# Optimization experiments

Hardware: AMD Instinct MI355X
Metric: run time of the kernel (lower is better)

The kernel has to match this reference:

```python
import jax, jax.numpy as jnp
import numpy as np

TARGET_RADIUS = 0.95
EPS = 1e-8

def _spectral_norm_wh(W_h, u):
    # Power iteration (3 steps) is done under no_grad in the original torch code,
    # so u, v are constants w.r.t. differentiation.
    Ws = jax.lax.stop_gradient(W_h)
    v = None
    for _ in range(3):
        v = Ws.T @ u
        v = v / (jnp.linalg.norm(v) + EPS)
        u = Ws @ v
        u = u / (jnp.linalg.norm(u) + EPS)
    sigma = jnp.abs(u @ W_h @ v)  # gradient flows through W_h here
    return W_h * (TARGET_RADIUS / (sigma + EPS))


def setup_inputs() -> dict:
    key = jax.random.key(0)
    kx, kwx, kwh, ku = jax.random.split(key, 4)
    T, B, D = 2048, 8, 1024
    x = jax.random.normal(kx, (T, B, D), dtype=jnp.float32)
    h0 = jnp.zeros((B, D), dtype=jnp.float32)
    W_x = jax.random.normal(kwx, (D, D), dtype=jnp.float32) * 0.02
    W_h = jax.random.normal(kwh, (D, D), dtype=jnp.float32) * (1.0 / np.sqrt(D))
    b = jnp.zeros((D,), dtype=jnp.float32)
    u = jax.random.normal(ku, (D,), dtype=jnp.float32)
    u = u / jnp.linalg.norm(u)
    return {"x": x, "h0": h0, "W_x": W_x, "W_h": W_h, "b": b, "u": u}


def reference(x, h0, W_x, W_h, b, u):
    # x: [T, B, D], h0: [B, D]
    Wh = _spectral_norm_wh(W_h, u)
    # Input projection is independent of the recurrence: one big GEMM.
    pre = jnp.einsum('tbd,ed->tbe', x, W_x) + b  # [T, B, D]

    def step(h_prev, p_t):
        h_new = p_t + h_prev @ Wh.T  # linear recurrence, no tanh
        return h_new, h_new

    _, hs = jax.lax.scan(step, h0, pre)  # hs: [T, B, D]
    h_all = jnp.concatenate([h0[None], hs], axis=0)  # [T+1, B, D]
    output = hs * (hs * jax.nn.sigmoid(hs))  # h * silu(h)
    return output, h_all
```

## Files before the change

kernel.cpp:

```cpp
#include <hip/hip_runtime.h>
#include <hip/hip_bf16.h>

#define DEV __device__ __forceinline__

typedef __bf16 bf16x8 __attribute__((ext_vector_type(8)));
typedef float  f32x4  __attribute__((ext_vector_type(4)));
typedef unsigned short u16;

DEV u16   f2b(float f) { __bf16 h = (__bf16)f; return __builtin_bit_cast(u16, h); }
DEV float b2f(u16 x)   { return __builtin_bit_cast(float, ((unsigned)x) << 16); }

DEV void gl_lds16(const u16* g, u16* l) {
  __builtin_amdgcn_global_load_lds((const __attribute__((address_space(1))) void*)g,
                                   (__attribute__((address_space(3))) void*)l, 16, 0, 0);
}

DEV long arow(int m, int S, int j) {
  if (S > 0)  return ((long)((m >> 3) * S + j)) * 8 + (m & 7);
  if (S == 0) return m;
  return m & 7;
}

struct ZCfg {
  const u16 *A0, *A1, *A2, *A3, *A4;
  const u16 *B0, *B1, *B2, *B3, *B4;
  int S0, J0, S1, J1, S2, J2, S3, J3, S4, J4;
  int nseg, mvalid, q, mode, ylim;
  const float* addc;
  const float* addf;
  const u16*   addb; int addS, addJ;
  float* outf;
  u16 *outb, *outbT, *outlo;
  u16* outm; int oS, oJ;
  u16 *glamH, *glamL;
  float *hall, *out0;
};
struct GArgs { ZCfg z0, z1, z2, z3; };

__global__ __launch_bounds__(256) void gU(GArgs ga)
{
  ZCfg c;
  switch (blockIdx.z) { case 0: c = ga.z0; break; case 1: c = ga.z1; break;
                        case 2: c = ga.z2; break; default: c = ga.z3; break; }

  int gx = gridDim.x;
  int fid = blockIdx.y * gx + blockIdx.x;
  int nwg = gx * gridDim.y;
  int idx = (c.ylim == (int)gridDim.y) ? ((fid & 7) * (nwg >> 3) + (fid >> 3))
                                       : fid;
  int mt = idx / gx, et = idx % gx;
  if (mt >= c.ylim) return;
  int m0 = mt << 6, e0 = et << 6;

  const int K = c.nseg << 10;
  int tid = threadIdx.x, lane = tid & 63, w = tid >> 6;
  int wrow = (w >> 1) << 5, wcol = (w & 1) << 5;

  __shared__ u16 As[2][8192], Bs[2][8192];
  f32x4 acc[2][2] = {};

  int rA[4], cA[4];
#pragma unroll
  for (int j = 0; j < 4; ++j) {
    int p = (j * 4 + w) * 1024 + lane * 16;
    int r = p >> 8, o = (p & 255) ^ ((r & 7) << 4);
    rA[j] = r; cA[j] = o >> 1;
  }
  auto seg = [&](int i, const u16*& A, int& S, int& J, const u16*& B) {
    switch (i) {
      case 0: A = c.A0; S = c.S0; J = c.J0; B = c.B0; break;
      case 1: A = c.A1; S = c.S1; J = c.J1; B = c.B1; break;
      case 2: A = c.A2; S = c.S2; J = c.J2; B = c.B2; break;
      case 3: A = c.A3; S = c.S3; J = c.J3; B = c.B3; break;
      default: A = c.A4; S = c.S4; J = c.J4; B = c.B4; break;
    }
  };
  auto stage = [&](int buf, int kt) {
    int si = kt >> 10, kl = kt & 1023;
    const u16 *A, *B; int S, J;
    seg(si, A, S, J, B);
#pragma unroll
    for (int j = 0; j < 4; ++j) {
      int grow = m0 + rA[j];
      gl_lds16(A + arow(grow, S, J) * 1024 + kl + cA[j], &As[buf][(j * 4 + w) * 512]);
    }
#pragma unroll
    for (int j = 0; j < 4; ++j)
      gl_lds16(B + (size_t)(e0 + rA[j]) * 1024 + kl + cA[j], &Bs[buf][(j * 4 + w) * 512]);
  };

  stage(0, 0);
  asm volatile("s_waitcnt vmcnt(0)" ::: "memory");
  __syncthreads();

  int buf = 0;
  for (int kt = 0; kt < K; kt += 128, buf ^= 1) {
    if (kt + 128 < K) stage(buf ^ 1, kt + 128);
#pragma unroll
    for (int ks = 0; ks < 4; ++ks) {
      int oa = ks * 64 + ((lane >> 4) << 4);
      bf16x8 af[2], bf[2];
#pragma unroll
      for (int s = 0; s < 2; ++s) {
        int ra = wrow + s * 16 + (lane & 15);
        int rb = wcol + s * 16 + (lane & 15);
        af[s] = *(const bf16x8*)((const char*)&As[buf][0] + ra * 256 + (oa ^ ((ra & 7) << 4)));
        bf[s] = *(const bf16x8*)((const char*)&Bs[buf][0] + rb * 256 + (oa ^ ((rb & 7) << 4)));
      }
#pragma unroll
      for (int ms = 0; ms < 2; ++ms)
#pragma unroll
        for (int ns = 0; ns < 2; ++ns)
          acc[ms][ns] = __builtin_amdgcn_mfma_f32_16x16x32_bf16(af[ms], bf[ns], acc[ms][ns], 0, 0, 0);
    }
    asm volatile("s_waitcnt vmcnt(0)" ::: "memory");
    __syncthreads();
  }

  int l4 = ((lane >> 4) << 2), lc = lane & 15;
#pragma unroll
  for (int ms = 0; ms < 2; ++ms)
#pragma unroll
    for (int ns = 0; ns < 2; ++ns)
#pragma unroll
      for (int j = 0; j < 4; ++j) {
        int row = m0 + wrow + ms * 16 + l4 + j;
        int col = e0 + wcol + ns * 16 + lc;
        float v = acc[ms][ns][j];
        if (c.mode == 0) {
          u16 h = f2b(v);
          if (c.outb)  c.outb[(size_t)row * 1024 + col] = h;
          if (c.outbT) c.outbT[(size_t)col * 1024 + row] = h;
        } else if (c.mode == 2) {
          if (c.addc) v += c.addc[col];
          if (c.addb)      v += b2f(c.addb[arow(row, c.addS, c.addJ) * 1024 + col]);
          else if (c.addf) v += c.addf[arow(row, c.addS, c.addJ) * 1024 + col];
          if (row < c.mvalid) {
            if (c.outf) c.outf[(size_t)row * 1024 + col] = v;
            u16 hi = f2b(v);
            if (c.outb)  c.outb[(size_t)row * 1024 + col] = hi;
            if (c.outlo) c.outlo[(size_t)row * 1024 + col] = f2b(v - b2f(hi));
            if (c.outm)  c.outm[arow(row, c.oS, c.oJ) * 1024 + col] = hi;
            if (c.glamH && ((row >> 3) & 15) == 0) {
              int r2 = ((row >> 3) >> 4) * 8 + (row & 7);
              c.glamH[(size_t)r2 * 1024 + col] = hi;
              c.glamL[(size_t)r2 * 1024 + col] = f2b(v - b2f(hi));
            }
          }
        } else {
          v += b2f(c.addb[arow(row, c.addS, c.addJ) * 1024 + col]);
          int t = (row >> 3) * 4 + c.q, b = row & 7;
          c.hall[(size_t)t * 8192 + b * 1024 + col] = v;
          float sg = 1.f / (1.f + __expf(-v));
          c.out0[(size_t)(t - 1) * 8192 + b * 1024 + col] = v * v * sg;
          if (c.outb) c.outb[(size_t)row * 1024 + col] = f2b(v);
        }
      }
}

__global__ void k_init(const float* __restrict__ u_in, const float* __restrict__ h0,
                       float* __restrict__ u_cur, float* __restrict__ v_acc,
                       float* __restrict__ u_acc, float* __restrict__ hall0,
                       u16* __restrict__ bndSb, u16* __restrict__ bndSlo,
                       u16* __restrict__ bndb)
{
  int i = blockIdx.x * 256 + threadIdx.x;
  if (i < 1024) { u_cur[i] = u_in[i]; v_acc[i] = 0.f; u_acc[i] = 0.f; }
  if (i < 8192) {
    float h = h0[i];
    hall0[i] = h;
    u16 hi = f2b(h);
    bndSb[i] = hi;
    bndSlo[i] = f2b(h - b2f(hi));
    bndb[i] = hi;
  }
}

__global__ void k_v(const float* __restrict__ W, const float* __restrict__ u_cur,
                    float* __restrict__ v_acc)
{
  int d = blockIdx.x * 256 + threadIdx.x;
  int e0 = blockIdx.y * 64;
  float a = 0.f;
  for (int e = e0; e < e0 + 64; ++e) a += W[(size_t)e * 1024 + d] * u_cur[e];
  atomicAdd(&v_acc[d], a);
}

__global__ void k_u(const float* __restrict__ W, const float* __restrict__ v_cur,
                    float* __restrict__ u_acc)
{
  int lg = threadIdx.x & 15, ei = threadIdx.x >> 4;
  int e = blockIdx.y * 16 + ei;
  int d0 = blockIdx.x * 512;
  float a = 0.f;
  for (int i = 0; i < 32; ++i) { int d = d0 + lg + 16 * i; a += W[(size_t)e * 1024 + d] * v_cur[d]; }
#pragma unroll
  for (int m = 1; m < 16; m <<= 1) a += __shfl_xor(a, m);
  if (lg == 0) atomicAdd(&u_acc[e], a);
}

__global__ void k_norm(const float* __restrict__ acc, float* __restrict__ outv,
                       float* __restrict__ z1)
{
  __shared__ float red[16];
  int t = threadIdx.x;
  float x = acc[t];
  float ss = x * x;
#pragma unroll
  for (int m = 1; m < 64; m <<= 1) ss += __shfl_xor(ss, m);
  if ((t & 63) == 0) red[t >> 6] = ss;
  __syncthreads();
  if (t < 64) {
    float s = (t < 16) ? red[t] : 0.f;
#pragma unroll
    for (int m = 1; m < 16; m <<= 1) s += __shfl_xor(s, m);
    if (t == 0) red[0] = s;
  }
  __syncthreads();
  float nrm = sqrtf(red[0]) + 1e-8f;
  outv[t] = x / nrm;
  z1[t] = 0.f;
}

__global__ void k_sigma(const float* __restrict__ acc, float* __restrict__ scale)
{
  __shared__ float red[16];
  int t = threadIdx.x;
  float x = acc[t];
  float ss = x * x;
#pragma unroll
  for (int m = 1; m < 64; m <<= 1) ss += __shfl_xor(ss, m);
  if ((t & 63) == 0) red[t >> 6] = ss;
  __syncthreads();
  if (t < 64) {
    float s = (t < 16) ? red[t] : 0.f;
#pragma unroll
    for (int m = 1; m < 16; m <<= 1) s += __shfl_xor(s, m);
    if (t == 0) {
      float sigma = s / (sqrtf(s) + 1e-8f);
      scale[0] = 0.95f / (sigma + 1e-8f);
    }
  }
}

__global__ void k_prep(const float* __restrict__ Wh, const float* __restrict__ Wx,
                       const float* __restrict__ scale, u16* __restrict__ wh_b,
                       u16* __restrict__ whT, u16* __restrict__ wxb)
{
  int i = blockIdx.x * 256 + threadIdx.x;
  float s = scale[0];
  int e = i >> 10, d = i & 1023;
  u16 hw = f2b(Wh[i] * s);
  wh_b[i] = hw;
  whT[(size_t)d * 1024 + e] = hw;
  wxb[i] = f2b(Wx[i]);
}

__global__ void k_cvt(const float* __restrict__ in, u16* __restrict__ out, int n)
{
  int i = (blockIdx.x * 256 + threadIdx.x) * 4;
  if (i >= n) return;
  float4 v = *(const float4*)(in + i);
  ushort4 o;
  o.x = f2b(v.x); o.y = f2b(v.y); o.z = f2b(v.z); o.w = f2b(v.w);
  *(ushort4*)(out + i) = o;
}

static void setseg(ZCfg& z, int i, const u16* A, int S, int J, const u16* B) {
  switch (i) {
    case 0: z.A0 = A; z.S0 = S; z.J0 = J; z.B0 = B; break;
    case 1: z.A1 = A; z.S1 = S; z.J1 = J; z.B1 = B; break;
    case 2: z.A2 = A; z.S2 = S; z.J2 = J; z.B2 = B; break;
    case 3: z.A3 = A; z.S3 = S; z.J3 = J; z.B3 = B; break;
    default: z.A4 = A; z.S4 = S; z.J4 = J; z.B4 = B; break;
  }
}
static void setsq(ZCfg& z, const u16* A, const u16* B, u16* o, u16* oT) {
  z.A0 = A; z.S0 = 0; z.J0 = 0; z.B0 = B; z.nseg = 1;
  z.outb = o; z.outbT = oT; z.mode = 0; z.ylim = 16;
}

extern "C" void kernel_launch(void* const* d_in, const int* in_sizes, int n_in,
                              void* d_out, int out_size, void* d_ws, size_t ws_size,
                              hipStream_t stream)
{
  (void)in_sizes; (void)n_in; (void)out_size; (void)ws_size;
  const float* x  = (const float*)d_in[0];
  const float* h0 = (const float*)d_in[1];
  const float* Wx = (const float*)d_in[2];
  const float* Wh = (const float*)d_in[3];
  const float* bv = (const float*)d_in[4];
  const float* uv = (const float*)d_in[5];

  float* out0 = (float*)d_out;
  float* hall = out0 + 16777216;

  const size_t M1 = 1048576;
  char* ws = (char*)d_ws;
  u16*   pre_b = (u16*)(ws);
  u16*   wh_b  = (u16*)(ws + 32 * M1);
  u16*   bnd_b = (u16*)(ws + 34 * M1);
  u16*   lb0   = (u16*)(ws + 42 * M1);
  u16*   bndSb = (u16*)(ws + 50 * M1);
  u16*   bndSlo= (u16*)(ws + 50 * M1 + 524288);
  float* u_cur = (float*)(ws + 51 * M1);
  float* v_cur = u_cur + 1024;
  float* v_acc = u_cur + 2048;
  float* u_acc = u_cur + 3072;
  float* scale = u_cur + 4096;
  u16*   W2    = (u16*)(ws + 52 * M1);

  char* HBS = (char*)hall + 32768;
  u16*   xb   = (u16*)(HBS);
  float* lC   = (float*)(HBS);
  u16*   lCb  = (u16*)(HBS + 16 * M1);
  float* lamF = (float*)(HBS + 24 * M1);
  u16* lamH0  = (u16*)(HBS + 25 * M1);
  u16* lamH1  = (u16*)(HBS + 25 * M1 + 524288);
  u16* lamL0  = (u16*)(HBS + 26 * M1);
  u16* lamL1  = (u16*)(HBS + 26 * M1 + 524288);
  u16* pcH0   = (u16*)(HBS + 27 * M1);
  u16* pcH1   = (u16*)(HBS + 27 * M1 + 524288);
  u16* pcL0   = (u16*)(HBS + 28 * M1);
  u16* pcL1   = (u16*)(HBS + 28 * M1 + 524288);
  auto slot = [&](int k) { return (u16*)(HBS + 32 * M1 + (size_t)k * 2 * M1); };
  u16* whT  = slot(0);
  u16* wxb  = slot(1);
  u16* W2T  = slot(3);
  u16* W3   = slot(4);
  u16* W4   = slot(5);
  u16* W4T  = slot(6);
  u16* W8   = slot(7);
  u16* W8T  = slot(8);
  u16* W12  = slot(9);
  u16* W16  = slot(10);
  u16* W16T = slot(11);
  u16* W32  = slot(12);
  u16* W32T = slot(13);
  u16* W64  = slot(14);
  u16* W64T = slot(15);
  u16* W128 = W8T, *W128T = W16T, *W192 = whT, *W256 = wxb;

  k_init<<<32, 256, 0, stream>>>(uv, h0, u_cur, v_acc, u_acc, hall,
                                 bndSb, bndSlo, bnd_b);

  for (int it = 0; it < 3; ++it) {
    k_v<<<dim3(4, 16), 256, 0, stream>>>(Wh, u_cur, v_acc);
    k_norm<<<1, 1024, 0, stream>>>(v_acc, v_cur, u_acc);
    k_u<<<dim3(2, 64), 256, 0, stream>>>(Wh, v_cur, u_acc);
    if (it < 2) k_norm<<<1, 1024, 0, stream>>>(u_acc, u_cur, v_acc);
    else        k_sigma<<<1, 1024, 0, stream>>>(u_acc, scale);
  }
  k_prep<<<4096, 256, 0, stream>>>(Wh, Wx, scale, wh_b, whT, wxb);
  k_cvt<<<16384, 256, 0, stream>>>(x, xb, 16777216);

  { GArgs a{}; ZCfg& z = a.z0;
    setseg(z, 0, xb, 0, 0, wxb);
    z.nseg = 1; z.mode = 2; z.ylim = 256; z.mvalid = 16384;
    z.addc = bv; z.outb = pre_b;
    setsq(a.z1, wh_b, whT, W2, W2T);
    gU<<<dim3(16, 256, 2), 256, 0, stream>>>(a); }

  { GArgs a{}; setsq(a.z0, W2, whT, W3, nullptr); setsq(a.z1, W2, W2T, W4, W4T);
    gU<<<dim3(16, 16, 2), 256, 0, stream>>>(a); }

  { GArgs a{}; ZCfg& z = a.z0;
    setseg(z, 0, pre_b, 4, 0, W3);
    setseg(z, 1, pre_b, 4, 1, W2);
    setseg(z, 2, pre_b, 4, 2, wh_b);
    z.nseg = 3; z.mode = 2; z.ylim = 64; z.mvalid = 4096;
    z.addb = pre_b; z.addS = 4; z.addJ = 3;
    z.outf = lC; z.outb = lCb;
    z.glamH = lamH0; z.glamL = lamL0;
    setsq(a.z1, W4, W4T, W8, W8T);
    gU<<<dim3(16, 64, 2), 256, 0, stream>>>(a); }

  { GArgs a{}; setsq(a.z0, W8, W4T, W12, nullptr); setsq(a.z1, W8, W8T, W16, W16T);
    gU<<<dim3(16, 16, 2), 256, 0, stream>>>(a); }

  {
    const u16 *chH = lamH0, *chL = lamL0;
    int j0s[3] = {1, 5, 9};
    u16* nxH[3] = { lamH1, lamH0, lamH1 };
    u16* nxL[3] = { lamL1, lamL0, lamL1 };
    const u16* sqA[3] = { W16, W32, W64 };
    const u16* sqB[3] = { W16T, W32T, W64T };
    u16* sqO[3] = { W32, W64, W128 };
    u16* sqT[3] = { W32T, W64T, W128T };
    for (int i = 0; i < 3; ++i) {
      GArgs a{}; ZCfg& z = a.z0;
      setseg(z, 0, chH, 0, 0, W16); setseg(z, 1, chL, 0, 0, W16);
      setseg(z, 2, lCb, 16, j0s[i],     W12);
      setseg(z, 3, lCb, 16, j0s[i] + 1, W8);
      setseg(z, 4, lCb, 16, j0s[i] + 2, W4);
      z.nseg = 5; z.mode = 2; z.ylim = 4; z.mvalid = 256;
      z.addf = lC; z.addS = 16; z.addJ = j0s[i] + 3;
      z.outb = nxH[i]; z.outlo = nxL[i];
      setsq(a.z1, sqA[i], sqB[i], sqO[i], sqT[i]);
      gU<<<dim3(16, 16, 2), 256, 0, stream>>>(a);
      chH = nxH[i]; chL = nxL[i];
    }
    GArgs a{}; ZCfg& z = a.z0;
    setseg(z, 0, chH, 0, 0, W12); setseg(z, 1, chL, 0, 0, W12);
    setseg(z, 2, lCb, 16, 13, W8); setseg(z, 3, lCb, 16, 14, W4);
    z.nseg = 4; z.mode = 2; z.ylim = 4; z.mvalid = 256;
    z.addf = lC; z.addS = 16; z.addJ = 15;
    z.outf = lamF; z.outb = lamH0; z.outlo = lamL0;
    setsq(a.z1, W128, W64T, W192, nullptr);
    setsq(a.z2, W128, W128T, W256, nullptr);
    gU<<<dim3(16, 16, 3), 256, 0, stream>>>(a);
  }

  {
    const u16* w64s[4] = { W64, W128, W192, W256 };
    for (int sb2 = 0; sb2 < 32; sb2 += 4) {
      int zmax = (sb2 == 28) ? 3 : 4;
      GArgs a{};
      ZCfg* zs[4] = { &a.z0, &a.z1, &a.z2, &a.z3 };
      for (int zz = 1; zz <= zmax; ++zz) {
        ZCfg& z = *zs[zz - 1];
        setseg(z, 0, bndSb + (size_t)sb2 * 8192, -1, 0, w64s[zz - 1]);
        int ns = 1;
        for (int i = 0; i < zz - 1; ++i)
          setseg(z, ns++, lamH0 + (size_t)(sb2 + i) * 8192, -1, 0, w64s[zz - 2 - i]);
        z.nseg = ns; z.mode = 2; z.ylim = 1; z.mvalid = 8;
        z.addf = lamF + (size_t)(sb2 + zz - 1) * 8192; z.addS = -1;
        z.outb = bndSb + (size_t)(sb2 + zz) * 8192;
        z.outlo = bndSlo + (size_t)(sb2 + zz) * 8192;
        z.outm = bnd_b + (size_t)16 * (sb2 + zz) * 8192; z.oS = 0;
      }
      gU<<<dim3(16, 1, zmax), 256, 0, stream>>>(a);
    }
  }

  {
    const u16* w4s[4] = { W4, W8, W12, W16 };
    const u16* cinH[4] = { bndSb, pcH0, pcH1, pcH0 };
    const u16* cinL[4] = { bndSlo, pcL0, pcL1, pcL0 };
    u16* coutH[4] = { pcH0, pcH1, pcH0, nullptr };
    u16* coutL[4] = { pcL0, pcL1, pcL0, nullptr };
    for (int t4 = 0; t4 < 4; ++t4) {
      int jb = 4 * t4;
      int zmax = (t4 == 3) ? 3 : 4;
      GArgs a{};
      ZCfg* zs[4] = { &a.z0, &a.z1, &a.z2, &a.z3 };
      for (int zz = 1; zz <= zmax; ++zz) {
        ZCfg& z = *zs[zz - 1];
        setseg(z, 0, cinH[t4], 0, 0, w4s[zz - 1]);
        setseg(z, 1, cinL[t4], 0, 0, w4s[zz - 1]);
        int ns = 2;
        for (int i = 0; i < zz - 1; ++i)
          setseg(z, ns++, lCb, 16, jb + i, w4s[zz - 2 - i]);
        z.nseg = ns; z.mode = 2; z.ylim = 4; z.mvalid = 256;
        z.addf = lC; z.addS = 16; z.addJ = jb + zz - 1;
        z.outm = bnd_b; z.oS = 16; z.oJ = jb + zz;
        if (zz == 4) { z.outb = coutH[t4]; z.outlo = coutL[t4]; }
      }
      gU<<<dim3(16, 4, zmax), 256, 0, stream>>>(a);
    }
  }

  {
    const u16* chains[2] = { bnd_b, lb0 };
    u16* chouts[2] = { lb0, nullptr };
    for (int half = 0; half < 2; ++half) {
      int qa = 2 * half + 1;
      GArgs a{};
      { ZCfg& z = a.z0;
        setseg(z, 0, chains[half], 0, 0, wh_b);
        z.nseg = 1; z.mode = 3; z.ylim = 64; z.q = qa;
        z.addb = pre_b; z.addS = 4; z.addJ = qa - 1;
        z.hall = hall; z.out0 = out0; }
      { ZCfg& z = a.z1;
        setseg(z, 0, chains[half], 0, 0, W2);
        setseg(z, 1, pre_b, 4, qa - 1, wh_b);
        z.nseg = 2; z.mode = 3; z.ylim = 64; z.q = qa + 1;
        z.addb = pre_b; z.addS = 4; z.addJ = qa;
        z.hall = hall; z.out0 = out0;
        z.outb = chouts[half]; }
      gU<<<dim3(16, 64, 2), 256, 0, stream>>>(a);
    }
  }
}
```

Before: 1.116 ms.

## Enlarge GEMM tiles to 128x128 and drop LDS double buffering

The shared GEMM kernel moves from 64x64 block tiles to 128x128, with each wave computing a 64x64 sub-tile through a 4x4 grid of MFMAs. The K step shrinks from 128 to 64, and the double-buffered LDS staging becomes a single buffer loaded, synchronised and consumed each iteration. All launch grids and ylim values are halved to match. The aim is more operand reuse per LDS load and fewer blocks on the large GEMMs. In exchange, global loads no longer overlap with MFMA work, and the many small recurrence GEMMs now launch far fewer blocks, which may leave much of the GPU idle.

```diff
diff --git a/kernel.cpp b/kernel.cpp
--- a/kernel.cpp
+++ b/kernel.cpp
@@ -50,20 +50,20 @@
                                        : fid;
   int mt = idx / gx, et = idx % gx;
   if (mt >= c.ylim) return;
-  int m0 = mt << 6, e0 = et << 6;
+  int m0 = mt << 7, e0 = et << 7;
 
   const int K = c.nseg << 10;
   int tid = threadIdx.x, lane = tid & 63, w = tid >> 6;
-  int wrow = (w >> 1) << 5, wcol = (w & 1) << 5;
-
-  __shared__ u16 As[2][8192], Bs[2][8192];
-  f32x4 acc[2][2] = {};
+  int wr = (w >> 1) << 6, wc = (w & 1) << 6;
+
+  __shared__ u16 As[8192], Bs[8192];
+  f32x4 acc[4][4] = {};
 
   int rA[4], cA[4];
 #pragma unroll
   for (int j = 0; j < 4; ++j) {
-    int p = (j * 4 + w) * 1024 + lane * 16;
-    int r = p >> 8, o = (p & 255) ^ ((r & 7) << 4);
+    int p = j * 4096 + tid * 16;
+    int r = p >> 7, o = (p & 127) ^ ((r & 7) << 4);
     rA[j] = r; cA[j] = o >> 1;
   }
   auto seg = [&](int i, const u16*& A, int& S, int& J, const u16*& B) {
@@ -75,57 +75,53 @@
       default: A = c.A4; S = c.S4; J = c.J4; B = c.B4; break;
     }
   };
-  auto stage = [&](int buf, int kt) {
+  auto stage = [&](int kt) {
     int si = kt >> 10, kl = kt & 1023;
     const u16 *A, *B; int S, J;
     seg(si, A, S, J, B);
 #pragma unroll
     for (int j = 0; j < 4; ++j) {
       int grow = m0 + rA[j];
-      gl_lds16(A + arow(grow, S, J) * 1024 + kl + cA[j], &As[buf][(j * 4 + w) * 512]);
+      gl_lds16(A + arow(grow, S, J) * 1024 + kl + cA[j], &As[j * 2048 + w * 512]);
     }
 #pragma unroll
     for (int j = 0; j < 4; ++j)
-      gl_lds16(B + (size_t)(e0 + rA[j]) * 1024 + kl + cA[j], &Bs[buf][(j * 4 + w) * 512]);
+      gl_lds16(B + (size_t)(e0 + rA[j]) * 1024 + kl + cA[j], &Bs[j * 2048 + w * 512]);
   };
 
-  stage(0, 0);
-  asm volatile("s_waitcnt vmcnt(0)" ::: "memory");
-  __syncthreads();
-
-  int buf = 0;
-  for (int kt = 0; kt < K; kt += 128, buf ^= 1) {
-    if (kt + 128 < K) stage(buf ^ 1, kt + 128);
-#pragma unroll
-    for (int ks = 0; ks < 4; ++ks) {
-      int oa = ks * 64 + ((lane >> 4) << 4);
-      bf16x8 af[2], bf[2];
-#pragma unroll
-      for (int s = 0; s < 2; ++s) {
-        int ra = wrow + s * 16 + (lane & 15);
-        int rb = wcol + s * 16 + (lane & 15);
-        af[s] = *(const bf16x8*)((const char*)&As[buf][0] + ra * 256 + (oa ^ ((ra & 7) << 4)));
-        bf[s] = *(const bf16x8*)((const char*)&Bs[buf][0] + rb * 256 + (oa ^ ((rb & 7) << 4)));
-      }
-#pragma unroll
-      for (int ms = 0; ms < 2; ++ms)
-#pragma unroll
-        for (int ns = 0; ns < 2; ++ns)
-          acc[ms][ns] = __builtin_amdgcn_mfma_f32_16x16x32_bf16(af[ms], bf[ns], acc[ms][ns], 0, 0, 0);
-    }
+  for (int kt = 0; kt < K; kt += 64) {
+    stage(kt);
     asm volatile("s_waitcnt vmcnt(0)" ::: "memory");
     __syncthreads();
+#pragma unroll
+    for (int ks = 0; ks < 2; ++ks) {
+      int oa = ks * 64 + ((lane >> 4) << 4);
+      bf16x8 af[4], bf[4];
+#pragma unroll
+      for (int f = 0; f < 4; ++f) {
+        int ra = wr + f * 16 + (lane & 15);
+        int rb = wc + f * 16 + (lane & 15);
+        af[f] = *(const bf16x8*)((const char*)As + ra * 128 + (oa ^ ((ra & 7) << 4)));
+        bf[f] = *(const bf16x8*)((const char*)Bs + rb * 128 + (oa ^ ((rb & 7) << 4)));
+      }
+#pragma unroll
+      for (int ms = 0; ms < 4; ++ms)
+#pragma unroll
+        for (int ns = 0; ns < 4; ++ns)
+          acc[ms][ns] = __builtin_amdgcn_mfma_f32_16x16x32_bf16(af[ms], bf[ns], acc[ms][ns], 0, 0, 0);
+    }
+    __syncthreads();
   }
 
   int l4 = ((lane >> 4) << 2), lc = lane & 15;
 #pragma unroll
-  for (int ms = 0; ms < 2; ++ms)
-#pragma unroll
-    for (int ns = 0; ns < 2; ++ns)
+  for (int ms = 0; ms < 4; ++ms)
+#pragma unroll
+    for (int ns = 0; ns < 4; ++ns)
 #pragma unroll
       for (int j = 0; j < 4; ++j) {
-        int row = m0 + wrow + ms * 16 + l4 + j;
-        int col = e0 + wcol + ns * 16 + lc;
+        int row = m0 + wr + ms * 16 + l4 + j;
+        int col = e0 + wc + ns * 16 + lc;
         float v = acc[ms][ns][j];
         if (c.mode == 0) {
           u16 h = f2b(v);
@@ -277,7 +273,7 @@
 }
 static void setsq(ZCfg& z, const u16* A, const u16* B, u16* o, u16* oT) {
   z.A0 = A; z.S0 = 0; z.J0 = 0; z.B0 = B; z.nseg = 1;
-  z.outb = o; z.outbT = oT; z.mode = 0; z.ylim = 16;
+  z.outb = o; z.outbT = oT; z.mode = 0; z.ylim = 8;
 }
 
 extern "C" void kernel_launch(void* const* d_in, const int* in_sizes, int n_in,
@@ -356,27 +352,27 @@
 
   { GArgs a{}; ZCfg& z = a.z0;
     setseg(z, 0, xb, 0, 0, wxb);
-    z.nseg = 1; z.mode = 2; z.ylim = 256; z.mvalid = 16384;
+    z.nseg = 1; z.mode = 2; z.ylim = 128; z.mvalid = 16384;
     z.addc = bv; z.outb = pre_b;
     setsq(a.z1, wh_b, whT, W2, W2T);
-    gU<<<dim3(16, 256, 2), 256, 0, stream>>>(a); }
+    gU<<<dim3(8, 128, 2), 256, 0, stream>>>(a); }
 
   { GArgs a{}; setsq(a.z0, W2, whT, W3, nullptr); setsq(a.z1, W2, W2T, W4, W4T);
-    gU<<<dim3(16, 16, 2), 256, 0, stream>>>(a); }
+    gU<<<dim3(8, 8, 2), 256, 0, stream>>>(a); }
 
   { GArgs a{}; ZCfg& z = a.z0;
     setseg(z, 0, pre_b, 4, 0, W3);
     setseg(z, 1, pre_b, 4, 1, W2);
     setseg(z, 2, pre_b, 4, 2, wh_b);
-    z.nseg = 3; z.mode = 2; z.ylim = 64; z.mvalid = 4096;
+    z.nseg = 3; z.mode = 2; z.ylim = 32; z.mvalid = 4096;
     z.addb = pre_b; z.addS = 4; z.addJ = 3;
     z.outf = lC; z.outb = lCb;
     z.glamH = lamH0; z.glamL = lamL0;
     setsq(a.z1, W4, W4T, W8, W8T);
-    gU<<<dim3(16, 64, 2), 256, 0, stream>>>(a); }
+    gU<<<dim3(8, 32, 2), 256, 0, stream>>>(a); }
 
   { GArgs a{}; setsq(a.z0, W8, W4T, W12, nullptr); setsq(a.z1, W8, W8T, W16, W16T);
-    gU<<<dim3(16, 16, 2), 256, 0, stream>>>(a); }
+    gU<<<dim3(8, 8, 2), 256, 0, stream>>>(a); }
 
   {
     const u16 *chH = lamH0, *chL = lamL0;
@@ -393,22 +389,22 @@
       setseg(z, 2, lCb, 16, j0s[i],     W12);
       setseg(z, 3, lCb, 16, j0s[i] + 1, W8);
       setseg(z, 4, lCb, 16, j0s[i] + 2, W4);
-      z.nseg = 5; z.mode = 2; z.ylim = 4; z.mvalid = 256;
+      z.nseg = 5; z.mode = 2; z.ylim = 2; z.mvalid = 256;
       z.addf = lC; z.addS = 16; z.addJ = j0s[i] + 3;
       z.outb = nxH[i]; z.outlo = nxL[i];
       setsq(a.z1, sqA[i], sqB[i], sqO[i], sqT[i]);
-      gU<<<dim3(16, 16, 2), 256, 0, stream>>>(a);
+      gU<<<dim3(8, 8, 2), 256, 0, stream>>>(a);
       chH = nxH[i]; chL = nxL[i];
     }
     GArgs a{}; ZCfg& z = a.z0;
     setseg(z, 0, chH, 0, 0, W12); setseg(z, 1, chL, 0, 0, W12);
     setseg(z, 2, lCb, 16, 13, W8); setseg(z, 3, lCb, 16, 14, W4);
-    z.nseg = 4; z.mode = 2; z.ylim = 4; z.mvalid = 256;
+    z.nseg = 4; z.mode = 2; z.ylim = 2; z.mvalid = 256;
     z.addf = lC; z.addS = 16; z.addJ = 15;
     z.outf = lamF; z.outb = lamH0; z.outlo = lamL0;
     setsq(a.z1, W128, W64T, W192, nullptr);
     setsq(a.z2, W128, W128T, W256, nullptr);
-    gU<<<dim3(16, 16, 3), 256, 0, stream>>>(a);
+    gU<<<dim3(8, 8, 3), 256, 0, stream>>>(a);
   }
 
   {
@@ -429,7 +425,7 @@
         z.outlo = bndSlo + (size_t)(sb2 + zz) * 8192;
         z.outm = bnd_b + (size_t)16 * (sb2 + zz) * 8192; z.oS = 0;
       }
-      gU<<<dim3(16, 1, zmax), 256, 0, stream>>>(a);
+      gU<<<dim3(8, 1, zmax), 256, 0, stream>>>(a);
     }
   }
 
@@ -451,12 +447,12 @@
         int ns = 2;
         for (int i = 0; i < zz - 1; ++i)
           setseg(z, ns++, lCb, 16, jb + i, w4s[zz - 2 - i]);
-        z.nseg = ns; z.mode = 2; z.ylim = 4; z.mvalid = 256;
+        z.nseg = ns; z.mode = 2; z.ylim = 2; z.mvalid = 256;
         z.addf = lC; z.addS = 16; z.addJ = jb + zz - 1;
         z.outm = bnd_b; z.oS = 16; z.oJ = jb + zz;
         if (zz == 4) { z.outb = coutH[t4]; z.outlo = coutL[t4]; }
       }
-      gU<<<dim3(16, 4, zmax), 256, 0, stream>>>(a);
+      gU<<<dim3(8, 2, zmax), 256, 0, stream>>>(a);
     }
   }
 
@@ -468,17 +464,17 @@
       GArgs a{};
       { ZCfg& z = a.z0;
         setseg(z, 0, chains[half], 0, 0, wh_b);
-        z.nseg = 1; z.mode = 3; z.ylim = 64; z.q = qa;
+        z.nseg = 1; z.mode = 3; z.ylim = 32; z.q = qa;
         z.addb = pre_b; z.addS = 4; z.addJ = qa - 1;
         z.hall = hall; z.out0 = out0; }
       { ZCfg& z = a.z1;
         setseg(z, 0, chains[half], 0, 0, W2);
         setseg(z, 1, pre_b, 4, qa - 1, wh_b);
-        z.nseg = 2; z.mode = 3; z.ylim = 64; z.q = qa + 1;
+        z.nseg = 2; z.mode = 3; z.ylim = 32; z.q = qa + 1;
         z.addb = pre_b; z.addS = 4; z.addJ = qa;
         z.hall = hall; z.out0 = out0;
         z.outb = chouts[half]; }
-      gU<<<dim3(16, 64, 2), 256, 0, stream>>>(a);
-    }
-  }
-}
+      gU<<<dim3(8, 32, 2), 256, 0, stream>>>(a);
+    }
+  }
+}
```

Measured after the change: 1.958 ms. +75.5%, slower.
